# Kernel optimization log

Hardware: AMD Instinct MI355X
Metric: run time of the kernel (lower is better)

The kernel has to match this reference:

```python
import jax, jax.numpy as jnp
import numpy as np

N = 100000      # nodes
E = 1600000     # directed edges (avg degree 16)
IN, HID, OUT = 128, 128, 64


def setup_inputs() -> dict:
    key = jax.random.key(0)
    ks = jax.random.split(key, 6)
    x = jax.random.normal(ks[0], (N, IN), dtype=jnp.float32)
    edge_index = jax.random.randint(ks[1], (2, E), 0, N, dtype=jnp.int32)
    W1 = jax.random.normal(ks[2], (IN, HID), dtype=jnp.float32) * (1.0 / np.sqrt(IN))
    b1 = jax.random.normal(ks[3], (HID,), dtype=jnp.float32) * 0.01
    W2 = jax.random.normal(ks[4], (HID, OUT), dtype=jnp.float32) * (1.0 / np.sqrt(HID))
    b2 = jax.random.normal(ks[5], (OUT,), dtype=jnp.float32) * 0.01
    return {"x": x, "edge_index": edge_index, "W1": W1, "b1": b1, "W2": W2, "b2": b2}


def _gcn_norm(edge_index):
    # add self-loops, compute symmetric normalization deg^-1/2 A_hat deg^-1/2
    loop = jnp.arange(N, dtype=edge_index.dtype)
    row = jnp.concatenate([edge_index[0], loop])  # source
    col = jnp.concatenate([edge_index[1], loop])  # target
    deg = jax.ops.segment_sum(jnp.ones(row.shape[0], jnp.float32), col, num_segments=N)
    dinv = jnp.where(deg > 0, jax.lax.rsqrt(deg), 0.0)
    norm = dinv[row] * dinv[col]  # [E+N]
    return row, col, norm


def _gcn_conv(x, row, col, norm, W, b):
    h = x @ W                              # [N, out] dense transform first (fewer features moved)
    msg = h[row] * norm[:, None]           # gather over edges
    agg = jax.ops.segment_sum(msg, col, num_segments=N)  # scatter-add to targets
    return agg + b


def reference(x, edge_index, W1, b1, W2, b2):
    row, col, norm = _gcn_norm(edge_index)
    h = jax.nn.relu(_gcn_conv(x, row, col, norm, W1, b1))
    return _gcn_conv(h, row, col, norm, W2, b2)
```

## Files before the change

### kernel.cpp

```cpp
#include <hip/hip_runtime.h>

#define NN 100000
#define NE 1600000

#define BSH 9
#define BSZ 512
#define NBUK 196
#define CAP 12288
#define CHUNK 4096
#define EPT 16

typedef _Float16 hs8 __attribute__((ext_vector_type(8)));
typedef float f32x4 __attribute__((ext_vector_type(4)));
typedef float f32x2 __attribute__((ext_vector_type(2)));
#define MFMA16H(a, b, c) __builtin_amdgcn_mfma_f32_16x16x32_f16(a, b, c, 0, 0, 0)

static inline size_t alignup(size_t x) { return (x + 255) & ~(size_t)255; }

union h8u { uint4 q; _Float16 h[8]; };


__global__ __launch_bounds__(256) void k_bucket(const int* __restrict__ row, const int* __restrict__ col,
                                                int* __restrict__ gcur, uint* __restrict__ pr_pack,
                                                const float* __restrict__ W1, _Float16* __restrict__ WT1,
                                                const float* __restrict__ W2, _Float16* __restrict__ WT2,
                                                int nbB) {
  int b = (int)blockIdx.x, t = threadIdx.x;
  if (b >= nbB) {
    int w = b - nbB;
    if (w < 64) {
      int i = w * 256 + t;
      int k = i >> 7, c = i & 127;
      WT1[c * 128 + k] = (_Float16)W1[i];
    } else {
      int i = (w - 64) * 256 + t;
      int k = i >> 6, c = i & 63;
      WT2[c * 128 + k] = (_Float16)W2[i];
    }
    return;
  }
  __shared__ int cnt[NBUK];
  for (int i = t; i < NBUK; i += 256) cnt[i] = 0;
  __syncthreads();
  int e0 = b * CHUNK;
  uint rr[EPT]; int cc[EPT];
#pragma unroll
  for (int i = 0; i < EPT; i++) {
    int e = e0 + t + i * 256;
    bool ok = e < NE;
    cc[i] = ok ? col[e] : -1;
    rr[i] = ok ? (uint)row[e] : 0u;
  }
#pragma unroll
  for (int i = 0; i < EPT; i++)
    if (cc[i] >= 0) {
      uint rank = (uint)atomicAdd(&cnt[cc[i] >> BSH], 1);
      rr[i] |= rank << 17;
    }
  __syncthreads();
  for (int i = t; i < NBUK; i += 256) {
    int c = cnt[i];
    cnt[i] = c ? (i * CAP + atomicAdd(&gcur[i], c)) : 0;
  }
  __syncthreads();
#pragma unroll
  for (int i = 0; i < EPT; i++)
    if (cc[i] >= 0) {
      int p = cnt[cc[i] >> BSH] + (int)(rr[i] >> 17);
      pr_pack[p] = ((rr[i] & 0x1FFFFu) << BSH) | (uint)(cc[i] & (BSZ - 1));
    }
}


__device__ __forceinline__ void gemm128_body(const float* __restrict__ x, const _Float16* __restrict__ WT,
                                             unsigned char* __restrict__ t8, int bid) {
  int wave = threadIdx.x >> 6, lane = threadIdx.x & 63;
  int col0 = wave * 32;
  int lr = lane & 15;
  int lk = (lane >> 4) * 8;
  hs8 bfrag[2][4];
#pragma unroll
  for (int n = 0; n < 2; n++)
#pragma unroll
    for (int ks = 0; ks < 4; ks++)
      bfrag[n][ks] = *(const hs8*)&WT[(size_t)(col0 + n * 16 + lr) * 128 + ks * 32 + lk];
  int row0 = bid * 64;
#pragma unroll 1
  for (int mt = 0; mt < 4; mt++) {
    int r0 = row0 + mt * 16;
    if (r0 >= NN) return;
    const float* xr = x + (size_t)(r0 + lr) * 128 + lk;
    f32x4 acc[2] = {{0.f, 0.f, 0.f, 0.f}, {0.f, 0.f, 0.f, 0.f}};
#pragma unroll
    for (int ks = 0; ks < 4; ks++) {
      float4 a0 = *(const float4*)&xr[ks * 32];
      float4 a1 = *(const float4*)&xr[ks * 32 + 4];
      hs8 af;
      af[0] = (_Float16)a0.x; af[1] = (_Float16)a0.y;
      af[2] = (_Float16)a0.z; af[3] = (_Float16)a0.w;
      af[4] = (_Float16)a1.x; af[5] = (_Float16)a1.y;
      af[6] = (_Float16)a1.z; af[7] = (_Float16)a1.w;
      acc[0] = MFMA16H(af, bfrag[0][ks], acc[0]);
      acc[1] = MFMA16H(af, bfrag[1][ks], acc[1]);
    }
    int rbase = r0 + (lane >> 4) * 4;
#pragma unroll
    for (int n = 0; n < 2; n++)
#pragma unroll
      for (int r = 0; r < 4; r++) {
        uint e = (uint)__builtin_amdgcn_cvt_pk_fp8_f32(acc[n][r], acc[n][r], 0, false);
        t8[(size_t)(rbase + r) * 128 + col0 + n * 16 + lr] = (unsigned char)(e & 0xffu);
      }
  }
}


__global__ __launch_bounds__(256) void k_fbg(const uint* __restrict__ pr_pack, const int* __restrict__ gcur,
                                             int* __restrict__ deg, float* __restrict__ dinv,
                                             const float* __restrict__ x, const _Float16* __restrict__ WT,
                                             unsigned char* __restrict__ t8) {
  if ((int)blockIdx.x >= NBUK) {
    gemm128_body(x, WT, t8, (int)blockIdx.x - NBUK);
    return;
  }
  __shared__ int dc[BSZ];
  int t = threadIdx.x, b = blockIdx.x;
  for (int i = t; i < BSZ; i += 256) dc[i] = 0;
  __syncthreads();
  int s = b * CAP;
  int n = min(gcur[b], CAP);
  for (int i = t; i < n; i += 256) atomicAdd(&dc[pr_pack[s + i] & (BSZ - 1)], 1);
  __syncthreads();
  int nb0 = b << BSH;
  for (int i = t; i < BSZ; i += 256) {
    int node = nb0 + i;
    if (node < NN) {
      int d = dc[i] + 1;
      deg[node] = d;
      dinv[node] = rsqrtf((float)d);
    }
  }
}


__global__ __launch_bounds__(256) void k_bfill(const uint* __restrict__ pr_pack, const int* __restrict__ gcur,
                                               const int* __restrict__ deg, const float* __restrict__ dinv,
                                               int* __restrict__ gctl, int* __restrict__ offs,
                                               uint2* __restrict__ wcsr) {
  __shared__ int loff[BSZ];
  __shared__ int cur[BSZ];
  __shared__ float dl[BSZ];
  __shared__ int tsum[256];
  __shared__ int sbase;
  int t = threadIdx.x, b = blockIdx.x;
  int nb0 = b << BSH;
  int i0 = 2 * t, i1 = i0 + 1;
  int n0 = nb0 + i0, n1 = nb0 + i1;
  int d0 = (n0 < NN) ? deg[n0] : 0;
  int d1 = (n1 < NN) ? deg[n1] : 0;
  int v = d0 + d1;
  tsum[t] = v;
  __syncthreads();
  for (int d = 1; d < 256; d <<= 1) {
    int tmp = (t >= d) ? tsum[t - d] : 0;
    __syncthreads();
    tsum[t] += tmp;
    __syncthreads();
  }
  if (t == 255) sbase = atomicAdd(&gctl[0], tsum[255]);
  __syncthreads();
  int base = sbase + tsum[t] - v;
  float dv0 = (n0 < NN) ? dinv[n0] : 0.f;
  float dv1 = (n1 < NN) ? dinv[n1] : 0.f;
  loff[i0] = base;
  loff[i1] = base + d0;
  dl[i0] = dv0;
  dl[i1] = dv1;
  cur[i0] = 1;
  cur[i1] = 1;
  if (n0 < NN) {
    offs[n0] = base;
    wcsr[base] = make_uint2((uint)n0, __float_as_uint(dv0 * dv0));
  }
  if (n1 < NN) {
    offs[n1] = base + d0;
    wcsr[base + d0] = make_uint2((uint)n1, __float_as_uint(dv1 * dv1));
  }
  __syncthreads();
  int s = b * CAP;
  int n = min(gcur[b], CAP);
  for (int i = t; i < n; i += 256) {
    uint prk = pr_pack[s + i];
    int li = (int)(prk & (BSZ - 1));
    uint r = prk >> BSH;
    int p = atomicAdd(&cur[li], 1);
    wcsr[loff[li] + p] = make_uint2(r, __float_as_uint(dinv[r] * dl[li]));
  }
}


__global__ __launch_bounds__(256) void k_gemm64(const _Float16* __restrict__ h, const _Float16* __restrict__ WT,
                                                _Float16* __restrict__ t2) {
  int wave = threadIdx.x >> 6, lane = threadIdx.x & 63;
  int col0 = wave * 16;
  int lr = lane & 15;
  int lk = (lane >> 4) * 8;
  hs8 bfrag[4];
#pragma unroll
  for (int ks = 0; ks < 4; ks++)
    bfrag[ks] = *(const hs8*)&WT[(size_t)(col0 + lr) * 128 + ks * 32 + lk];
  int row0 = blockIdx.x * 64;
#pragma unroll 1
  for (int mt = 0; mt < 4; mt++) {
    int r0 = row0 + mt * 16;
    if (r0 >= NN) return;
    const _Float16* hr = h + (size_t)(r0 + lr) * 128 + lk;
    f32x4 acc = {0.f, 0.f, 0.f, 0.f};
#pragma unroll
    for (int ks = 0; ks < 4; ks++) {
      hs8 af = *(const hs8*)&hr[ks * 32];
      acc = MFMA16H(af, bfrag[ks], acc);
    }
    int rbase = r0 + (lane >> 4) * 4;
#pragma unroll
    for (int r = 0; r < 4; r++)
      t2[(size_t)(rbase + r) * 64 + col0 + lr] = (_Float16)acc[r];
  }
}


__global__ __launch_bounds__(256) void k_agg128(const unsigned char* __restrict__ t8, const int* __restrict__ offs,
                                                const int* __restrict__ deg, const uint2* __restrict__ wcsr,
                                                const float* __restrict__ bias, _Float16* __restrict__ out) {
  int wave = threadIdx.x >> 6, lane = threadIdx.x & 63;
  int half = lane >> 5;
  int sub = (lane >> 4) & 1;
  int f = lane & 15;
  int node = blockIdx.x * 8 + wave * 2 + half;
  int beg = offs[node];
  int d = deg[node];
  const char* tb = (const char*)t8;
  float acc[8] = {};
  int trips = (d + 1) >> 1;
  uint2 e = (sub < d) ? wcsr[beg + sub] : make_uint2(0u, 0u);
#pragma unroll 1
  for (int k = 0; k < trips; k++) {
    int ns = (k + 1) * 2 + sub;
    uint2 en = (ns < d) ? wcsr[beg + ns] : make_uint2(0u, 0u);
    float s = __uint_as_float(e.y);
    uint2 u = *(const uint2*)(tb + (((size_t)e.x) << 7) + (f << 3));
    f32x2 p0 = __builtin_amdgcn_cvt_pk_f32_fp8(u.x, false);
    f32x2 p1 = __builtin_amdgcn_cvt_pk_f32_fp8(u.x, true);
    f32x2 p2 = __builtin_amdgcn_cvt_pk_f32_fp8(u.y, false);
    f32x2 p3 = __builtin_amdgcn_cvt_pk_f32_fp8(u.y, true);
    acc[0] = fmaf(p0[0], s, acc[0]);
    acc[1] = fmaf(p0[1], s, acc[1]);
    acc[2] = fmaf(p1[0], s, acc[2]);
    acc[3] = fmaf(p1[1], s, acc[3]);
    acc[4] = fmaf(p2[0], s, acc[4]);
    acc[5] = fmaf(p2[1], s, acc[5]);
    acc[6] = fmaf(p3[0], s, acc[6]);
    acc[7] = fmaf(p3[1], s, acc[7]);
    e = en;
  }
#pragma unroll
  for (int j = 0; j < 8; j++) acc[j] += __shfl_xor(acc[j], 16);
  if (sub == 0) {
    float4 b0 = *(const float4*)&bias[f * 8];
    float4 b1 = *(const float4*)&bias[f * 8 + 4];
    h8u st;
    st.h[0] = (_Float16)fmaxf(acc[0] + b0.x, 0.f);
    st.h[1] = (_Float16)fmaxf(acc[1] + b0.y, 0.f);
    st.h[2] = (_Float16)fmaxf(acc[2] + b0.z, 0.f);
    st.h[3] = (_Float16)fmaxf(acc[3] + b0.w, 0.f);
    st.h[4] = (_Float16)fmaxf(acc[4] + b1.x, 0.f);
    st.h[5] = (_Float16)fmaxf(acc[5] + b1.y, 0.f);
    st.h[6] = (_Float16)fmaxf(acc[6] + b1.z, 0.f);
    st.h[7] = (_Float16)fmaxf(acc[7] + b1.w, 0.f);
    *(uint4*)&out[(size_t)node * 128 + f * 8] = st.q;
  }
}

__global__ __launch_bounds__(256) void k_agg64(const _Float16* __restrict__ t, const int* __restrict__ offs,
                                               const int* __restrict__ deg, const uint2* __restrict__ wcsr,
                                               const float* __restrict__ bias, float* __restrict__ out) {
  int wave = threadIdx.x >> 6, lane = threadIdx.x & 63;
  int half = lane >> 5;
  int sub = (lane >> 3) & 3;
  int f8 = lane & 7;
  int node = blockIdx.x * 8 + wave * 2 + half;
  int beg = offs[node];
  int d = deg[node];
  const char* tb = (const char*)t;
  float acc[8] = {};
  int trips = (d + 3) >> 2;
  uint2 e = (sub < d) ? wcsr[beg + sub] : make_uint2(0u, 0u);
#pragma unroll 1
  for (int k = 0; k < trips; k++) {
    int ns = (k + 1) * 4 + sub;
    uint2 en = (ns < d) ? wcsr[beg + ns] : make_uint2(0u, 0u);
    float s = __uint_as_float(e.y);
    h8u u;
    u.q = *(const uint4*)(tb + (((size_t)e.x) << 7) + (f8 << 4));
    acc[0] = fmaf((float)u.h[0], s, acc[0]);
    acc[1] = fmaf((float)u.h[1], s, acc[1]);
    acc[2] = fmaf((float)u.h[2], s, acc[2]);
    acc[3] = fmaf((float)u.h[3], s, acc[3]);
    acc[4] = fmaf((float)u.h[4], s, acc[4]);
    acc[5] = fmaf((float)u.h[5], s, acc[5]);
    acc[6] = fmaf((float)u.h[6], s, acc[6]);
    acc[7] = fmaf((float)u.h[7], s, acc[7]);
    e = en;
  }
#pragma unroll
  for (int j = 0; j < 8; j++) {
    acc[j] += __shfl_xor(acc[j], 8);
    acc[j] += __shfl_xor(acc[j], 16);
  }
  if (sub == 0) {
    float4 b0 = *(const float4*)&bias[f8 * 8];
    float4 b1 = *(const float4*)&bias[f8 * 8 + 4];
    float4 o0 = make_float4(acc[0] + b0.x, acc[1] + b0.y, acc[2] + b0.z, acc[3] + b0.w);
    float4 o1 = make_float4(acc[4] + b1.x, acc[5] + b1.y, acc[6] + b1.z, acc[7] + b1.w);
    *(float4*)&out[(size_t)node * 64 + f8 * 8] = o0;
    *(float4*)&out[(size_t)node * 64 + f8 * 8 + 4] = o1;
  }
}


extern "C" void kernel_launch(void* const* d_in, const int* in_sizes, int n_in,
                              void* d_out, int out_size, void* d_ws, size_t ws_size,
                              hipStream_t stream) {
  const float* x  = (const float*)d_in[0];
  const int*   ei = (const int*)d_in[1];
  const float* W1 = (const float*)d_in[2];
  const float* b1 = (const float*)d_in[3];
  const float* W2 = (const float*)d_in[4];
  const float* b2 = (const float*)d_in[5];
  float* out = (float*)d_out;

  char* p = (char*)d_ws;
  int* gcur      = (int*)p;      p += alignup((size_t)NBUK * 4);
  int* gctl      = (int*)p;      p += alignup(256);
  int* deg       = (int*)p;      p += alignup((size_t)NN * 4);
  int* offs      = (int*)p;      p += alignup((size_t)NN * 4);
  float* dinv    = (float*)p;    p += alignup((size_t)NN * 4);
  uint2* wcsr    = (uint2*)p;    p += alignup((size_t)(NE + NN + 64) * 8);
  _Float16* WT1  = (_Float16*)p; p += alignup(128 * 128 * 2);
  _Float16* WT2  = (_Float16*)p; p += alignup(64 * 128 * 2);
  unsigned char* t8 = (unsigned char*)p; p += alignup((size_t)NN * 128);
  _Float16* t2   = (_Float16*)p; p += alignup((size_t)NN * 64 * 2);
  _Float16* h1   = (_Float16*)p; p += alignup((size_t)NN * 128 * 2);
  uint* pr_pack  = (uint*)t2;
  (void)ws_size; (void)in_sizes; (void)n_in; (void)out_size;

  const int* row = ei;
  const int* col = ei + NE;

  int nbB = (NE + CHUNK - 1) / CHUNK;
  int nbG = (NN + 63) / 64;
  int nbA = NN / 8;

  hipMemsetAsync(gcur, 0, alignup((size_t)NBUK * 4) + 256, stream);
  k_bucket<<<nbB + 96, 256, 0, stream>>>(row, col, gcur, pr_pack, W1, WT1, W2, WT2, nbB);
  k_fbg<<<NBUK + nbG, 256, 0, stream>>>(pr_pack, gcur, deg, dinv, x, WT1, t8);
  k_bfill<<<NBUK, 256, 0, stream>>>(pr_pack, gcur, deg, dinv, gctl, offs, wcsr);
  k_agg128<<<nbA, 256, 0, stream>>>(t8, offs, deg, wcsr, b1, h1);
  k_gemm64<<<nbG, 256, 0, stream>>>(h1, WT2, t2);
  k_agg64<<<nbA, 256, 0, stream>>>(t2, offs, deg, wcsr, b2, out);
}
```

Baseline: 185.2 us.

## Pack CSR edge weights into 32-bit words and split GEMM across fill kernels

Edge entries shrink from an 8-byte (index, float) pair to one 32-bit word: a 17-bit node index plus a bf16-rounded 15-bit weight (sign bit dropped). This halves the CSR bytes read by both aggregation kernels. The first-layer GEMM blocks are now split between the degree-count kernel and the CSR-fill kernel, so the GEMM overlaps the fill. The bucketing kernel also doubles its chunk size, keeps only the column in registers and reads the row later. In exchange, edge weights lose precision, and the packing relies on node indices fitting in 17 bits and weights being positive.

Result: slower. 203.0 us (+9.6%).

```diff
diff --git a/kernel.cpp b/kernel.cpp
--- a/kernel.cpp
+++ b/kernel.cpp
@@ -7,8 +7,9 @@
 #define BSZ 512
 #define NBUK 196
 #define CAP 12288
-#define CHUNK 4096
-#define EPT 16
+#define CHUNK 8192
+#define EPT 32
+#define GSPLIT 781
 
 typedef _Float16 hs8 __attribute__((ext_vector_type(8)));
 typedef float f32x4 __attribute__((ext_vector_type(4)));
@@ -19,15 +20,23 @@
 
 union h8u { uint4 q; _Float16 h[8]; };
 
+__device__ __forceinline__ uint packw(uint r, float w) {
+  uint wb = __float_as_uint(w);
+  wb = (wb + 0x7fffu + ((wb >> 16) & 1u)) >> 16;
+  return (wb << 17) | r;
+}
+__device__ __forceinline__ float unpw(uint e) {
+  return __uint_as_float((e & 0xFFFE0000u) >> 1);
+}
+
 
 __global__ __launch_bounds__(256) void k_bucket(const int* __restrict__ row, const int* __restrict__ col,
                                                 int* __restrict__ gcur, uint* __restrict__ pr_pack,
                                                 const float* __restrict__ W1, _Float16* __restrict__ WT1,
-                                                const float* __restrict__ W2, _Float16* __restrict__ WT2,
-                                                int nbB) {
+                                                const float* __restrict__ W2, _Float16* __restrict__ WT2) {
   int b = (int)blockIdx.x, t = threadIdx.x;
-  if (b >= nbB) {
-    int w = b - nbB;
+  if (b >= NBUK) {
+    int w = b - NBUK;
     if (w < 64) {
       int i = w * 256 + t;
       int k = i >> 7, c = i & 127;
@@ -43,19 +52,17 @@
   for (int i = t; i < NBUK; i += 256) cnt[i] = 0;
   __syncthreads();
   int e0 = b * CHUNK;
-  uint rr[EPT]; int cc[EPT];
+  uint cc[EPT];
 #pragma unroll
   for (int i = 0; i < EPT; i++) {
     int e = e0 + t + i * 256;
-    bool ok = e < NE;
-    cc[i] = ok ? col[e] : -1;
-    rr[i] = ok ? (uint)row[e] : 0u;
+    cc[i] = (e < NE) ? (uint)col[e] : 0xFFFFFFFFu;
   }
 #pragma unroll
   for (int i = 0; i < EPT; i++)
-    if (cc[i] >= 0) {
+    if (cc[i] != 0xFFFFFFFFu) {
       uint rank = (uint)atomicAdd(&cnt[cc[i] >> BSH], 1);
-      rr[i] |= rank << 17;
+      cc[i] |= rank << 17;
     }
   __syncthreads();
   for (int i = t; i < NBUK; i += 256) {
@@ -65,9 +72,12 @@
   __syncthreads();
 #pragma unroll
   for (int i = 0; i < EPT; i++)
-    if (cc[i] >= 0) {
-      int p = cnt[cc[i] >> BSH] + (int)(rr[i] >> 17);
-      pr_pack[p] = ((rr[i] & 0x1FFFFu) << BSH) | (uint)(cc[i] & (BSZ - 1));
+    if (cc[i] != 0xFFFFFFFFu) {
+      int e = e0 + t + i * 256;
+      uint r = (uint)row[e];
+      uint c17 = cc[i] & 0x1FFFFu;
+      int p = cnt[c17 >> BSH] + (int)(cc[i] >> 17);
+      pr_pack[p] = (r << BSH) | (c17 & (BSZ - 1));
     }
 }
 
@@ -115,10 +125,10 @@
 }
 
 
-__global__ __launch_bounds__(256) void k_fbg(const uint* __restrict__ pr_pack, const int* __restrict__ gcur,
-                                             int* __restrict__ deg, float* __restrict__ dinv,
-                                             const float* __restrict__ x, const _Float16* __restrict__ WT,
-                                             unsigned char* __restrict__ t8) {
+__global__ __launch_bounds__(256) void k_fA(const uint* __restrict__ pr_pack, const int* __restrict__ gcur,
+                                            int* __restrict__ deg, float* __restrict__ dinv,
+                                            const float* __restrict__ x, const _Float16* __restrict__ WT,
+                                            unsigned char* __restrict__ t8) {
   if ((int)blockIdx.x >= NBUK) {
     gemm128_body(x, WT, t8, (int)blockIdx.x - NBUK);
     return;
@@ -143,10 +153,16 @@
 }
 
 
-__global__ __launch_bounds__(256) void k_bfill(const uint* __restrict__ pr_pack, const int* __restrict__ gcur,
-                                               const int* __restrict__ deg, const float* __restrict__ dinv,
-                                               int* __restrict__ gctl, int* __restrict__ offs,
-                                               uint2* __restrict__ wcsr) {
+__global__ __launch_bounds__(256) void k_fB(const uint* __restrict__ pr_pack, const int* __restrict__ gcur,
+                                            const int* __restrict__ deg, const float* __restrict__ dinv,
+                                            int* __restrict__ gctl, int* __restrict__ offs,
+                                            uint* __restrict__ wcsr,
+                                            const float* __restrict__ x, const _Float16* __restrict__ WT,
+                                            unsigned char* __restrict__ t8) {
+  if ((int)blockIdx.x >= NBUK) {
+    gemm128_body(x, WT, t8, (int)blockIdx.x - NBUK + GSPLIT);
+    return;
+  }
   __shared__ int loff[BSZ];
   __shared__ int cur[BSZ];
   __shared__ float dl[BSZ];
@@ -180,11 +196,11 @@
   cur[i1] = 1;
   if (n0 < NN) {
     offs[n0] = base;
-    wcsr[base] = make_uint2((uint)n0, __float_as_uint(dv0 * dv0));
+    wcsr[base] = packw((uint)n0, dv0 * dv0);
   }
   if (n1 < NN) {
     offs[n1] = base + d0;
-    wcsr[base + d0] = make_uint2((uint)n1, __float_as_uint(dv1 * dv1));
+    wcsr[base + d0] = packw((uint)n1, dv1 * dv1);
   }
   __syncthreads();
   int s = b * CAP;
@@ -194,7 +210,7 @@
     int li = (int)(prk & (BSZ - 1));
     uint r = prk >> BSH;
     int p = atomicAdd(&cur[li], 1);
-    wcsr[loff[li] + p] = make_uint2(r, __float_as_uint(dinv[r] * dl[li]));
+    wcsr[loff[li] + p] = packw(r, dinv[r] * dl[li]);
   }
 }
 
@@ -230,7 +246,7 @@
 
 
 __global__ __launch_bounds__(256) void k_agg128(const unsigned char* __restrict__ t8, const int* __restrict__ offs,
-                                                const int* __restrict__ deg, const uint2* __restrict__ wcsr,
+                                                const int* __restrict__ deg, const uint* __restrict__ wcsr,
                                                 const float* __restrict__ bias, _Float16* __restrict__ out) {
   int wave = threadIdx.x >> 6, lane = threadIdx.x & 63;
   int half = lane >> 5;
@@ -242,13 +258,13 @@
   const char* tb = (const char*)t8;
   float acc[8] = {};
   int trips = (d + 1) >> 1;
-  uint2 e = (sub < d) ? wcsr[beg + sub] : make_uint2(0u, 0u);
+  uint e = (sub < d) ? wcsr[beg + sub] : 0u;
 #pragma unroll 1
   for (int k = 0; k < trips; k++) {
     int ns = (k + 1) * 2 + sub;
-    uint2 en = (ns < d) ? wcsr[beg + ns] : make_uint2(0u, 0u);
-    float s = __uint_as_float(e.y);
-    uint2 u = *(const uint2*)(tb + (((size_t)e.x) << 7) + (f << 3));
+    uint en = (ns < d) ? wcsr[beg + ns] : 0u;
+    float s = unpw(e);
+    uint2 u = *(const uint2*)(tb + (((size_t)(e & 0x1FFFFu)) << 7) + (f << 3));
     f32x2 p0 = __builtin_amdgcn_cvt_pk_f32_fp8(u.x, false);
     f32x2 p1 = __builtin_amdgcn_cvt_pk_f32_fp8(u.x, true);
     f32x2 p2 = __builtin_amdgcn_cvt_pk_f32_fp8(u.y, false);
@@ -282,7 +298,7 @@
 }
 
 __global__ __launch_bounds__(256) void k_agg64(const _Float16* __restrict__ t, const int* __restrict__ offs,
-                                               const int* __restrict__ deg, const uint2* __restrict__ wcsr,
+                                               const int* __restrict__ deg, const uint* __restrict__ wcsr,
                                                const float* __restrict__ bias, float* __restrict__ out) {
   int wave = threadIdx.x >> 6, lane = threadIdx.x & 63;
   int half = lane >> 5;
@@ -294,14 +310,14 @@
   const char* tb = (const char*)t;
   float acc[8] = {};
   int trips = (d + 3) >> 2;
-  uint2 e = (sub < d) ? wcsr[beg + sub] : make_uint2(0u, 0u);
+  uint e = (sub < d) ? wcsr[beg + sub] : 0u;
 #pragma unroll 1
   for (int k = 0; k < trips; k++) {
     int ns = (k + 1) * 4 + sub;
-    uint2 en = (ns < d) ? wcsr[beg + ns] : make_uint2(0u, 0u);
-    float s = __uint_as_float(e.y);
+    uint en = (ns < d) ? wcsr[beg + ns] : 0u;
+    float s = unpw(e);
     h8u u;
-    u.q = *(const uint4*)(tb + (((size_t)e.x) << 7) + (f8 << 4));
+    u.q = *(const uint4*)(tb + (((size_t)(e & 0x1FFFFu)) << 7) + (f8 << 4));
     acc[0] = fmaf((float)u.h[0], s, acc[0]);
     acc[1] = fmaf((float)u.h[1], s, acc[1]);
     acc[2] = fmaf((float)u.h[2], s, acc[2]);
@@ -345,7 +361,7 @@
   int* deg       = (int*)p;      p += alignup((size_t)NN * 4);
   int* offs      = (int*)p;      p += alignup((size_t)NN * 4);
   float* dinv    = (float*)p;    p += alignup((size_t)NN * 4);
-  uint2* wcsr    = (uint2*)p;    p += alignup((size_t)(NE + NN + 64) * 8);
+  uint* wcsr     = (uint*)p;     p += alignup((size_t)(NE + NN + 64) * 4);
   _Float16* WT1  = (_Float16*)p; p += alignup(128 * 128 * 2);
   _Float16* WT2  = (_Float16*)p; p += alignup(64 * 128 * 2);
   unsigned char* t8 = (unsigned char*)p; p += alignup((size_t)NN * 128);
@@ -357,14 +373,13 @@
   const int* row = ei;
   const int* col = ei + NE;
 
-  int nbB = (NE + CHUNK - 1) / CHUNK;
   int nbG = (NN + 63) / 64;
   int nbA = NN / 8;
 
   hipMemsetAsync(gcur, 0, alignup((size_t)NBUK * 4) + 256, stream);
-  k_bucket<<<nbB + 96, 256, 0, stream>>>(row, col, gcur, pr_pack, W1, WT1, W2, WT2, nbB);
-  k_fbg<<<NBUK + nbG, 256, 0, stream>>>(pr_pack, gcur, deg, dinv, x, WT1, t8);
-  k_bfill<<<NBUK, 256, 0, stream>>>(pr_pack, gcur, deg, dinv, gctl, offs, wcsr);
+  k_bucket<<<NBUK + 96, 256, 0, stream>>>(row, col, gcur, pr_pack, W1, WT1, W2, WT2);
+  k_fA<<<NBUK + GSPLIT, 256, 0, stream>>>(pr_pack, gcur, deg, dinv, x, WT1, t8);
+  k_fB<<<NBUK + (nbG - GSPLIT), 256, 0, stream>>>(pr_pack, gcur, deg, dinv, gctl, offs, wcsr, x, WT1, t8);
   k_agg128<<<nbA, 256, 0, stream>>>(t8, offs, deg, wcsr, b1, h1);
   k_gemm64<<<nbG, 256, 0, stream>>>(h1, WT2, t2);
   k_agg64<<<nbA, 256, 0, stream>>>(t2, offs, deg, wcsr, b2, out);
```
